# Kernel optimization log

Measured on AMD Instinct MI355X. Metric: run time of the kernel, lower is better.

## Reference

```python
import jax, jax.numpy as jnp
import numpy as np

N_NODES = 50000
N_EDGES = 800000
D_IN = 64
D_OUT = 64


def setup_inputs() -> dict:
    key = jax.random.key(0)
    k1, k2, k3, k4, k5, k6 = jax.random.split(key, 6)
    feat = jax.random.normal(k1, (N_NODES, D_IN), dtype=jnp.float32)
    edge_weight = jax.random.uniform(k2, (N_EDGES, 1), dtype=jnp.float32)
    # xavier_uniform bound for [D_IN, D_OUT]
    bound = float(np.sqrt(6.0 / (D_IN + D_OUT)))
    W1 = jax.random.uniform(k3, (D_IN, D_OUT), minval=-bound, maxval=bound, dtype=jnp.float32)
    W2 = jax.random.uniform(k4, (D_IN, D_OUT), minval=-bound, maxval=bound, dtype=jnp.float32)
    src = jax.random.randint(k5, (N_EDGES,), 0, N_NODES, dtype=jnp.int64)
    dst = jax.random.randint(k6, (N_EDGES,), 0, N_NODES, dtype=jnp.int64)
    return {"feat": feat, "edge_weight": edge_weight, "W1": W1, "W2": W2, "src": src, "dst": dst}


def reference(feat, edge_weight, W1, W2, src, dst):
    # message: u_sub_e -> src feature minus (broadcast) edge weight  [E, D_IN]
    msgs = feat[src] - edge_weight
    # sum aggregation over destination nodes  [N, D_IN]
    agg = jax.ops.segment_sum(msgs, dst, num_segments=feat.shape[0])
    # dual dense projections; no activation (activation=None)
    rst = jnp.matmul(feat, W1) + jnp.matmul(agg, W2)
    return rst
```

## Files before the change

### kernel.cpp

```cpp
#include <hip/hip_runtime.h>

#define NN 50000
#define NE 800000
#define D  64
#define NB 782
#define EBLK 2048
#define NEB 391
#define CAPB 1280
#define CONVB 1563

typedef unsigned int u32;
typedef unsigned short u16;
typedef unsigned long long u64;
typedef __attribute__((ext_vector_type(8))) short bf16x8;
typedef __attribute__((ext_vector_type(4))) float f32x4;
typedef __attribute__((ext_vector_type(2))) float f32x2;

__device__ __forceinline__ int wave_incl_scan(int v, int lane) {
    #pragma unroll
    for (int off = 1; off < 64; off <<= 1) {
        int t = __shfl_up(v, off);
        if (lane >= off) v += t;
    }
    return v;
}

__device__ __forceinline__ u32 f2bf(float x) {
    u32 u = __float_as_uint(x);
    return (u + 0x7fffu + ((u >> 16) & 1u)) >> 16;
}

__device__ __forceinline__ bf16x8 as_bf8(uint4 u) {
    union { uint4 a; bf16x8 b; } x; x.a = u; return x.b;
}

__device__ __forceinline__ u32 pk_fp8x4(float a, float b, float c, float d) {
    int w = __builtin_amdgcn_cvt_pk_fp8_f32(a, b, 0, false);
    w = __builtin_amdgcn_cvt_pk_fp8_f32(c, d, w, true);
    return (u32)w;
}

__global__ __launch_bounds__(256) void convz_kernel(const float* __restrict__ feat,
                                                    uint4* __restrict__ featb,
                                                    uint2* __restrict__ featb8,
                                                    u32* __restrict__ cursor)
{
    int tid = threadIdx.x;
    if (blockIdx.x == CONVB) {
        for (int i = tid; i < NB; i += 256) cursor[i] = 0;
        return;
    }
    int i = blockIdx.x * 256 + tid;
    if (i >= NN * D / 8) return;
    const float4* f4 = (const float4*)feat;
    float4 a = f4[2 * i], b = f4[2 * i + 1];
    uint4 o;
    o.x = f2bf(a.x) | (f2bf(a.y) << 16);
    o.y = f2bf(a.z) | (f2bf(a.w) << 16);
    o.z = f2bf(b.x) | (f2bf(b.y) << 16);
    o.w = f2bf(b.z) | (f2bf(b.w) << 16);
    featb[i] = o;
    uint2 p8;
    p8.x = pk_fp8x4(a.x, a.y, a.z, a.w);
    p8.y = pk_fp8x4(b.x, b.y, b.z, b.w);
    featb8[i] = p8;
}

__global__ __launch_bounds__(256) void kb_scatter(const int* __restrict__ src,
                                                  const int* __restrict__ dst,
                                                  const float* __restrict__ ew,
                                                  u32* __restrict__ cursor,
                                                  u64* __restrict__ sorted)
{
    __shared__ u32 h[NB], eb[NB], ctr[NB], gb[NB];
    __shared__ u64 buf[EBLK];
    int tid = threadIdx.x;
    for (int i = tid; i < NB; i += 256) h[i] = 0;
    __syncthreads();
    int base = blockIdx.x * EBLK;
    int n = min(EBLK, NE - base);

    u32 rd[8], rs[8], rw[8];
    #pragma unroll
    for (int j = 0; j < 8; ++j) {
        int k = tid + j * 256;
        if (k < n) {
            int e = base + k;
            rd[j] = (u32)dst[e];
            rs[j] = (u32)src[e];
            rw[j] = __float_as_uint(ew[e]);
            atomicAdd(&h[rd[j] >> 6], 1u);
        }
    }
    __syncthreads();
    if (tid < 64) {
        u32 carry = 0;
        for (int c = 0; c < 13; ++c) {
            int idx = c * 64 + tid;
            u32 v = (idx < NB) ? h[idx] : 0;
            int incl = wave_incl_scan((int)v, tid);
            if (idx < NB) { u32 e = (u32)incl - v + carry; eb[idx] = e; ctr[idx] = e; }
            carry += (u32)__shfl(incl, 63);
        }
    }
    __syncthreads();
    for (int i = tid; i < NB; i += 256) gb[i] = atomicAdd(&cursor[i], h[i]);
    __syncthreads();
    #pragma unroll
    for (int j = 0; j < 8; ++j) {
        int k = tid + j * 256;
        if (k < n) {
            u64 rec = ((u64)((rd[j] << 16) | rs[j]) << 32) | (u64)rw[j];
            u32 p = atomicAdd(&ctr[rd[j] >> 6], 1u);
            buf[p] = rec;
        }
    }
    __syncthreads();
    for (int k = tid; k < n; k += 256) {
        u64 rec = buf[k];
        u32 bin = (u32)(rec >> 54);
        u32 idx = gb[bin] + (u32)k - eb[bin];
        if (idx < CAPB) sorted[(size_t)bin * CAPB + idx] = rec;
    }
}

__global__ __launch_bounds__(1024) void kcg_sortgather(
    const u64* __restrict__ sorted,
    const u32* __restrict__ cursor,
    const u32* __restrict__ fb8,
    uint2* __restrict__ aggb,
    float* __restrict__ sW)
{
    __shared__ u32 hcnt[64], hbase[65], ctr[64];
    __shared__ u16 bufS[CAPB];
    __shared__ u32 bufWf[CAPB];
    int tid = threadIdx.x;
    int bin = blockIdx.x;
    int n = min((int)cursor[bin], CAPB);
    const size_t rbase = (size_t)bin * CAPB;

    if (tid < 64) hcnt[tid] = 0;
    __syncthreads();
    for (int k = tid; k < n; k += 1024)
        atomicAdd(&hcnt[(int)(sorted[rbase + k] >> 48) & 63], 1u);
    __syncthreads();
    if (tid < 64) {
        u32 v = hcnt[tid];
        int incl = wave_incl_scan((int)v, tid);
        u32 ex = (u32)incl - v;
        hbase[tid] = ex; ctr[tid] = ex;
        if (tid == 63) hbase[64] = (u32)incl;
    }
    __syncthreads();
    for (int k = tid; k < n; k += 1024) {
        u64 rec = sorted[rbase + k];
        u32 p = atomicAdd(&ctr[(int)(rec >> 48) & 63], 1u);
        bufS[p]  = (u16)(rec >> 32);
        bufWf[p] = (u32)rec;
    }
    __syncthreads();

    const int w    = tid >> 6;
    const int lane = tid & 63;
    const int g    = lane >> 4;
    const int li   = lane & 15;
    const int ln   = w * 4 + g;
    const int node = (bin << 6) + ln;
    if (node >= NN) return;

    int e   = (int)hbase[ln];
    int end = (int)hbase[ln + 1];

    if (li == 0) {
        float s = 0.f;
        for (int j = e; j < end; ++j) s += __uint_as_float(bufWf[j]);
        sW[node] = s;
    }

    float4 acc = make_float4(0.f, 0.f, 0.f, 0.f);
    for (; e + 7 < end; e += 8) {
        int s0 = bufS[e],     s1 = bufS[e + 1];
        int s2 = bufS[e + 2], s3 = bufS[e + 3];
        int s4 = bufS[e + 4], s5 = bufS[e + 5];
        int s6 = bufS[e + 6], s7 = bufS[e + 7];
        u32 u0 = fb8[(size_t)s0 * 16 + li];
        u32 u1 = fb8[(size_t)s1 * 16 + li];
        u32 u2 = fb8[(size_t)s2 * 16 + li];
        u32 u3 = fb8[(size_t)s3 * 16 + li];
        u32 u4 = fb8[(size_t)s4 * 16 + li];
        u32 u5 = fb8[(size_t)s5 * 16 + li];
        u32 u6 = fb8[(size_t)s6 * 16 + li];
        u32 u7 = fb8[(size_t)s7 * 16 + li];
        #pragma unroll
        for (int j = 0; j < 8; ++j) {
            u32 uu = j == 0 ? u0 : j == 1 ? u1 : j == 2 ? u2 : j == 3 ? u3
                   : j == 4 ? u4 : j == 5 ? u5 : j == 6 ? u6 : u7;
            f32x2 lo = __builtin_amdgcn_cvt_pk_f32_fp8((int)uu, false);
            f32x2 hi = __builtin_amdgcn_cvt_pk_f32_fp8((int)uu, true);
            acc.x += lo.x; acc.y += lo.y; acc.z += hi.x; acc.w += hi.y;
        }
    }
    for (; e < end; ++e) {
        u32 uu = fb8[(size_t)bufS[e] * 16 + li];
        f32x2 lo = __builtin_amdgcn_cvt_pk_f32_fp8((int)uu, false);
        f32x2 hi = __builtin_amdgcn_cvt_pk_f32_fp8((int)uu, true);
        acc.x += lo.x; acc.y += lo.y; acc.z += hi.x; acc.w += hi.y;
    }

    uint2 o;
    o.x = f2bf(acc.x) | (f2bf(acc.y) << 16);
    o.y = f2bf(acc.z) | (f2bf(acc.w) << 16);
    aggb[(size_t)node * 16 + li] = o;
}

__global__ __launch_bounds__(256) void gemm_mfma(
    const uint4* __restrict__ featb,
    const uint4* __restrict__ aggb,
    const float* __restrict__ sW,
    const float* __restrict__ W1,
    const float* __restrict__ W2,
    float* __restrict__ out)
{
    __shared__ u16 wT[64][136];
    __shared__ float csp[4][64];
    __shared__ float csum[64];
    const int tid = threadIdx.x;

    for (int i = tid; i < 8192; i += 256) {
        int k = i >> 6, c = i & 63;
        float v = (k < 64) ? W1[i] : W2[i - 4096];
        wT[c][k] = (u16)f2bf(v);
    }
    {
        int c = tid & 63, kq = tid >> 6;
        float s = 0.f;
        for (int k = kq * 16; k < kq * 16 + 16; ++k) s += W2[k * 64 + c];
        csp[kq][c] = s;
    }
    __syncthreads();
    if (tid < 64) csum[tid] = csp[0][tid] + csp[1][tid] + csp[2][tid] + csp[3][tid];
    __syncthreads();

    int gw = blockIdx.x * 4 + (tid >> 6);
    if (gw >= NN / 16) return;
    const int l  = tid & 63;
    const int lr = l & 15;
    const int q  = l >> 4;

    bf16x8 b[4][4];
    #pragma unroll
    for (int nt = 0; nt < 4; ++nt)
        #pragma unroll
        for (int kk = 0; kk < 4; ++kk)
            b[nt][kk] = *(const bf16x8*)&wT[nt * 16 + lr][kk * 32 + q * 8];

    const int m0 = gw * 16;
    const size_t arow = (size_t)(m0 + lr) * 8;
    bf16x8 a0 = as_bf8(featb[arow + q]);
    bf16x8 a1 = as_bf8(featb[arow + 4 + q]);
    bf16x8 a2 = as_bf8(aggb[arow + q]);
    bf16x8 a3 = as_bf8(aggb[arow + 4 + q]);

    f32x4 acc0 = {0.f, 0.f, 0.f, 0.f};
    f32x4 acc1 = acc0, acc2 = acc0, acc3 = acc0;

    acc0 = __builtin_amdgcn_mfma_f32_16x16x32_bf16(a0, b[0][0], acc0, 0, 0, 0);
    acc1 = __builtin_amdgcn_mfma_f32_16x16x32_bf16(a0, b[1][0], acc1, 0, 0, 0);
    acc2 = __builtin_amdgcn_mfma_f32_16x16x32_bf16(a0, b[2][0], acc2, 0, 0, 0);
    acc3 = __builtin_amdgcn_mfma_f32_16x16x32_bf16(a0, b[3][0], acc3, 0, 0, 0);

    acc0 = __builtin_amdgcn_mfma_f32_16x16x32_bf16(a1, b[0][1], acc0, 0, 0, 0);
    acc1 = __builtin_amdgcn_mfma_f32_16x16x32_bf16(a1, b[1][1], acc1, 0, 0, 0);
    acc2 = __builtin_amdgcn_mfma_f32_16x16x32_bf16(a1, b[2][1], acc2, 0, 0, 0);
    acc3 = __builtin_amdgcn_mfma_f32_16x16x32_bf16(a1, b[3][1], acc3, 0, 0, 0);

    acc0 = __builtin_amdgcn_mfma_f32_16x16x32_bf16(a2, b[0][2], acc0, 0, 0, 0);
    acc1 = __builtin_amdgcn_mfma_f32_16x16x32_bf16(a2, b[1][2], acc1, 0, 0, 0);
    acc2 = __builtin_amdgcn_mfma_f32_16x16x32_bf16(a2, b[2][2], acc2, 0, 0, 0);
    acc3 = __builtin_amdgcn_mfma_f32_16x16x32_bf16(a2, b[3][2], acc3, 0, 0, 0);

    acc0 = __builtin_amdgcn_mfma_f32_16x16x32_bf16(a3, b[0][3], acc0, 0, 0, 0);
    acc1 = __builtin_amdgcn_mfma_f32_16x16x32_bf16(a3, b[1][3], acc1, 0, 0, 0);
    acc2 = __builtin_amdgcn_mfma_f32_16x16x32_bf16(a3, b[2][3], acc2, 0, 0, 0);
    acc3 = __builtin_amdgcn_mfma_f32_16x16x32_bf16(a3, b[3][3], acc3, 0, 0, 0);

    float4 sw4 = *(const float4*)&sW[m0 + q * 4];
    const float* swp = (const float*)&sw4;

    #pragma unroll
    for (int r = 0; r < 4; ++r) {
        size_t rowoff = (size_t)(m0 + q * 4 + r) * D;
        float s = swp[r];
        out[rowoff +  0 + lr] = acc0[r] - s * csum[ 0 + lr];
        out[rowoff + 16 + lr] = acc1[r] - s * csum[16 + lr];
        out[rowoff + 32 + lr] = acc2[r] - s * csum[32 + lr];
        out[rowoff + 48 + lr] = acc3[r] - s * csum[48 + lr];
    }
}

extern "C" void kernel_launch(void* const* d_in, const int* in_sizes, int n_in,
                              void* d_out, int out_size, void* d_ws, size_t ws_size,
                              hipStream_t stream)
{
    const float* feat = (const float*)d_in[0];
    const float* ew   = (const float*)d_in[1];
    const float* W1   = (const float*)d_in[2];
    const float* W2   = (const float*)d_in[3];
    const int*   src  = (const int*)  d_in[4];
    const int*   dst  = (const int*)  d_in[5];
    float* out = (float*)d_out;

    char* p = (char*)d_ws;
    size_t o = 0;
    auto take = [&](size_t bytes) { char* q = p + o; o = (o + bytes + 255) & ~(size_t)255; return q; };
    u64* sorted  = (u64*)take((size_t)NB * CAPB * 8);
    u32* cursor  = (u32*)take((size_t)NB * 4);
    uint4* featb = (uint4*)take((size_t)NN * D * 2);
    uint2* featb8= (uint2*)take((size_t)NN * D);
    uint4* aggb  = (uint4*)take((size_t)NN * D * 2);
    float* sW    = (float*)take((size_t)NN * 4 + 256);

    convz_kernel  <<<CONVB + 1, 256, 0, stream>>>(feat, featb, featb8, cursor);
    kb_scatter    <<<NEB, 256, 0, stream>>>(src, dst, ew, cursor, sorted);
    kcg_sortgather<<<NB, 1024, 0, stream>>>(sorted, cursor, (const u32*)featb8,
                                            (uint2*)aggb, sW);
    gemm_mfma     <<<(NN / 16 + 3) / 4, 256, 0, stream>>>(featb, aggb, sW, W1, W2, out);
}
```

Before: 57.63 us.

## Fuse sort-gather aggregation with MFMA projection into one kernel

Merges the gather/aggregate kernel with the dense dual-projection GEMM. Aggregated rows now stay in shared memory as bf16 and feed MFMA directly, so the global aggb and sW buffers and one kernel launch go away. Each of the 16 waves in a 1024-thread block computes one 16x16 output tile. The cost is that every block now transposes and converts W1/W2 into LDS, and the larger LDS footprint may reduce occupancy. The early return for out-of-range nodes is removed and the feature buffer is padded so the last bin reads safely.

Result: faster. 56.37 us (-2.2%).

```diff
diff --git a/kernel.cpp b/kernel.cpp
--- a/kernel.cpp
+++ b/kernel.cpp
@@ -124,23 +124,43 @@
     }
 }
 
-__global__ __launch_bounds__(1024) void kcg_sortgather(
+__global__ __launch_bounds__(1024) void kcgg(
     const u64* __restrict__ sorted,
     const u32* __restrict__ cursor,
     const u32* __restrict__ fb8,
-    uint2* __restrict__ aggb,
-    float* __restrict__ sW)
+    const uint4* __restrict__ featb,
+    const float* __restrict__ W1,
+    const float* __restrict__ W2,
+    float* __restrict__ out)
 {
     __shared__ u32 hcnt[64], hbase[65], ctr[64];
     __shared__ u16 bufS[CAPB];
     __shared__ u32 bufWf[CAPB];
-    int tid = threadIdx.x;
-    int bin = blockIdx.x;
-    int n = min((int)cursor[bin], CAPB);
+    __shared__ u16 aggT[64][72];
+    __shared__ u16 wT[64][136];
+    __shared__ float csp[4][64];
+    __shared__ float csum[64];
+    __shared__ float sWs[64];
+
+    const int tid = threadIdx.x;
+    const int bin = blockIdx.x;
+    const int n = min((int)cursor[bin], CAPB);
     const size_t rbase = (size_t)bin * CAPB;
 
+    for (int i = tid; i < 8192; i += 1024) {
+        int k = i >> 6, c = i & 63;
+        float v = (k < 64) ? W1[i] : W2[i - 4096];
+        wT[c][k] = (u16)f2bf(v);
+    }
+    if (tid < 256) {
+        int c = tid & 63, kq = tid >> 6;
+        float s = 0.f;
+        for (int k = kq * 16; k < kq * 16 + 16; ++k) s += W2[k * 64 + c];
+        csp[kq][c] = s;
+    }
     if (tid < 64) hcnt[tid] = 0;
     __syncthreads();
+    if (tid < 64) csum[tid] = csp[0][tid] + csp[1][tid] + csp[2][tid] + csp[3][tid];
     for (int k = tid; k < n; k += 1024)
         atomicAdd(&hcnt[(int)(sorted[rbase + k] >> 48) & 63], 1u);
     __syncthreads();
@@ -165,8 +185,6 @@
     const int g    = lane >> 4;
     const int li   = lane & 15;
     const int ln   = w * 4 + g;
-    const int node = (bin << 6) + ln;
-    if (node >= NN) return;
 
     int e   = (int)hbase[ln];
     int end = (int)hbase[ln + 1];
@@ -174,7 +192,7 @@
     if (li == 0) {
         float s = 0.f;
         for (int j = e; j < end; ++j) s += __uint_as_float(bufWf[j]);
-        sW[node] = s;
+        sWs[ln] = s;
     }
 
     float4 acc = make_float4(0.f, 0.f, 0.f, 0.f);
@@ -206,95 +224,44 @@
         f32x2 hi = __builtin_amdgcn_cvt_pk_f32_fp8((int)uu, true);
         acc.x += lo.x; acc.y += lo.y; acc.z += hi.x; acc.w += hi.y;
     }
-
-    uint2 o;
-    o.x = f2bf(acc.x) | (f2bf(acc.y) << 16);
-    o.y = f2bf(acc.z) | (f2bf(acc.w) << 16);
-    aggb[(size_t)node * 16 + li] = o;
-}
-
-__global__ __launch_bounds__(256) void gemm_mfma(
-    const uint4* __restrict__ featb,
-    const uint4* __restrict__ aggb,
-    const float* __restrict__ sW,
-    const float* __restrict__ W1,
-    const float* __restrict__ W2,
-    float* __restrict__ out)
-{
-    __shared__ u16 wT[64][136];
-    __shared__ float csp[4][64];
-    __shared__ float csum[64];
-    const int tid = threadIdx.x;
-
-    for (int i = tid; i < 8192; i += 256) {
-        int k = i >> 6, c = i & 63;
-        float v = (k < 64) ? W1[i] : W2[i - 4096];
-        wT[c][k] = (u16)f2bf(v);
-    }
     {
-        int c = tid & 63, kq = tid >> 6;
-        float s = 0.f;
-        for (int k = kq * 16; k < kq * 16 + 16; ++k) s += W2[k * 64 + c];
-        csp[kq][c] = s;
-    }
-    __syncthreads();
-    if (tid < 64) csum[tid] = csp[0][tid] + csp[1][tid] + csp[2][tid] + csp[3][tid];
-    __syncthreads();
-
-    int gw = blockIdx.x * 4 + (tid >> 6);
-    if (gw >= NN / 16) return;
-    const int l  = tid & 63;
-    const int lr = l & 15;
-    const int q  = l >> 4;
-
-    bf16x8 b[4][4];
-    #pragma unroll
-    for (int nt = 0; nt < 4; ++nt)
-        #pragma unroll
-        for (int kk = 0; kk < 4; ++kk)
-            b[nt][kk] = *(const bf16x8*)&wT[nt * 16 + lr][kk * 32 + q * 8];
-
-    const int m0 = gw * 16;
+        uint2 o;
+        o.x = f2bf(acc.x) | (f2bf(acc.y) << 16);
+        o.y = f2bf(acc.z) | (f2bf(acc.w) << 16);
+        *(uint2*)&aggT[ln][li * 4] = o;
+    }
+    __syncthreads();
+
+    const int nt = w >> 2;
+    const int ct = w & 3;
+    const int lr = lane & 15;
+    const int q  = lane >> 4;
+    const int m0 = (bin << 6) + nt * 16;
+
+    bf16x8 b0 = *(const bf16x8*)&wT[ct * 16 + lr][ 0 + q * 8];
+    bf16x8 b1 = *(const bf16x8*)&wT[ct * 16 + lr][32 + q * 8];
+    bf16x8 b2 = *(const bf16x8*)&wT[ct * 16 + lr][64 + q * 8];
+    bf16x8 b3 = *(const bf16x8*)&wT[ct * 16 + lr][96 + q * 8];
+
     const size_t arow = (size_t)(m0 + lr) * 8;
     bf16x8 a0 = as_bf8(featb[arow + q]);
     bf16x8 a1 = as_bf8(featb[arow + 4 + q]);
-    bf16x8 a2 = as_bf8(aggb[arow + q]);
-    bf16x8 a3 = as_bf8(aggb[arow + 4 + q]);
-
-    f32x4 acc0 = {0.f, 0.f, 0.f, 0.f};
-    f32x4 acc1 = acc0, acc2 = acc0, acc3 = acc0;
-
-    acc0 = __builtin_amdgcn_mfma_f32_16x16x32_bf16(a0, b[0][0], acc0, 0, 0, 0);
-    acc1 = __builtin_amdgcn_mfma_f32_16x16x32_bf16(a0, b[1][0], acc1, 0, 0, 0);
-    acc2 = __builtin_amdgcn_mfma_f32_16x16x32_bf16(a0, b[2][0], acc2, 0, 0, 0);
-    acc3 = __builtin_amdgcn_mfma_f32_16x16x32_bf16(a0, b[3][0], acc3, 0, 0, 0);
-
-    acc0 = __builtin_amdgcn_mfma_f32_16x16x32_bf16(a1, b[0][1], acc0, 0, 0, 0);
-    acc1 = __builtin_amdgcn_mfma_f32_16x16x32_bf16(a1, b[1][1], acc1, 0, 0, 0);
-    acc2 = __builtin_amdgcn_mfma_f32_16x16x32_bf16(a1, b[2][1], acc2, 0, 0, 0);
-    acc3 = __builtin_amdgcn_mfma_f32_16x16x32_bf16(a1, b[3][1], acc3, 0, 0, 0);
-
-    acc0 = __builtin_amdgcn_mfma_f32_16x16x32_bf16(a2, b[0][2], acc0, 0, 0, 0);
-    acc1 = __builtin_amdgcn_mfma_f32_16x16x32_bf16(a2, b[1][2], acc1, 0, 0, 0);
-    acc2 = __builtin_amdgcn_mfma_f32_16x16x32_bf16(a2, b[2][2], acc2, 0, 0, 0);
-    acc3 = __builtin_amdgcn_mfma_f32_16x16x32_bf16(a2, b[3][2], acc3, 0, 0, 0);
-
-    acc0 = __builtin_amdgcn_mfma_f32_16x16x32_bf16(a3, b[0][3], acc0, 0, 0, 0);
-    acc1 = __builtin_amdgcn_mfma_f32_16x16x32_bf16(a3, b[1][3], acc1, 0, 0, 0);
-    acc2 = __builtin_amdgcn_mfma_f32_16x16x32_bf16(a3, b[2][3], acc2, 0, 0, 0);
-    acc3 = __builtin_amdgcn_mfma_f32_16x16x32_bf16(a3, b[3][3], acc3, 0, 0, 0);
-
-    float4 sw4 = *(const float4*)&sW[m0 + q * 4];
-    const float* swp = (const float*)&sw4;
+    bf16x8 a2 = *(const bf16x8*)&aggT[nt * 16 + lr][q * 8];
+    bf16x8 a3 = *(const bf16x8*)&aggT[nt * 16 + lr][32 + q * 8];
+
+    f32x4 o4 = {0.f, 0.f, 0.f, 0.f};
+    o4 = __builtin_amdgcn_mfma_f32_16x16x32_bf16(a0, b0, o4, 0, 0, 0);
+    o4 = __builtin_amdgcn_mfma_f32_16x16x32_bf16(a1, b1, o4, 0, 0, 0);
+    o4 = __builtin_amdgcn_mfma_f32_16x16x32_bf16(a2, b2, o4, 0, 0, 0);
+    o4 = __builtin_amdgcn_mfma_f32_16x16x32_bf16(a3, b3, o4, 0, 0, 0);
 
     #pragma unroll
     for (int r = 0; r < 4; ++r) {
-        size_t rowoff = (size_t)(m0 + q * 4 + r) * D;
-        float s = swp[r];
-        out[rowoff +  0 + lr] = acc0[r] - s * csum[ 0 + lr];
-        out[rowoff + 16 + lr] = acc1[r] - s * csum[16 + lr];
-        out[rowoff + 32 + lr] = acc2[r] - s * csum[32 + lr];
-        out[rowoff + 48 + lr] = acc3[r] - s * csum[48 + lr];
+        int row = m0 + q * 4 + r;
+        if (row < NN) {
+            float s = sWs[nt * 16 + q * 4 + r];
+            out[(size_t)row * D + ct * 16 + lr] = o4[r] - s * csum[ct * 16 + lr];
+        }
     }
 }
 
@@ -313,16 +280,13 @@
     char* p = (char*)d_ws;
     size_t o = 0;
     auto take = [&](size_t bytes) { char* q = p + o; o = (o + bytes + 255) & ~(size_t)255; return q; };
-    u64* sorted  = (u64*)take((size_t)NB * CAPB * 8);
-    u32* cursor  = (u32*)take((size_t)NB * 4);
-    uint4* featb = (uint4*)take((size_t)NN * D * 2);
-    uint2* featb8= (uint2*)take((size_t)NN * D);
-    uint4* aggb  = (uint4*)take((size_t)NN * D * 2);
-    float* sW    = (float*)take((size_t)NN * 4 + 256);
-
-    convz_kernel  <<<CONVB + 1, 256, 0, stream>>>(feat, featb, featb8, cursor);
-    kb_scatter    <<<NEB, 256, 0, stream>>>(src, dst, ew, cursor, sorted);
-    kcg_sortgather<<<NB, 1024, 0, stream>>>(sorted, cursor, (const u32*)featb8,
-                                            (uint2*)aggb, sW);
-    gemm_mfma     <<<(NN / 16 + 3) / 4, 256, 0, stream>>>(featb, aggb, sW, W1, W2, out);
-}
+    u64* sorted   = (u64*)take((size_t)NB * CAPB * 8);
+    u32* cursor   = (u32*)take((size_t)NB * 4);
+    uint4* featb  = (uint4*)take((size_t)NN * D * 2 + 8192);
+    uint2* featb8 = (uint2*)take((size_t)NN * D);
+
+    convz_kernel<<<CONVB + 1, 256, 0, stream>>>(feat, featb, featb8, cursor);
+    kb_scatter  <<<NEB, 256, 0, stream>>>(src, dst, ew, cursor, sorted);
+    kcgg        <<<NB, 1024, 0, stream>>>(sorted, cursor, (const u32*)featb8,
+                                          featb, W1, W2, out);
+}
```
